# Optimization experiments

Hardware: AMD Instinct MI355X
Metric: run time of the kernel (lower is better)

Reference implementation:

```python
import jax, jax.numpy as jnp
import numpy as np

T, B, H, EMB, EVO, A = 700, 32, 800, 32, 21, 60
DIN = EMB + EVO            # 53 = embedding + evolutionary profile
RNN_OUT = 2 * H + DIN      # 1653 = bi-LSTM output + skip connection

BOND_LENGTHS = jnp.array([145.801, 152.326, 132.868], jnp.float32)
BOND_ANGLES = jnp.array([2.124, 1.941, 2.028], jnp.float32)
INIT_MAT = jnp.array([[-np.sqrt(0.5), np.sqrt(1.5), 0.0],
                      [-np.sqrt(2.0), 0.0, 0.0],
                      [0.0, 0.0, 0.0]], jnp.float32)


def setup_inputs():
    key = jax.random.key(0)
    ks = jax.random.split(key, 12)
    s = 0.03  # ~ pytorch LSTM uniform(-1/sqrt(H), 1/sqrt(H)) scale

    def lstm_params(k, d):
        k1, k2, k3 = jax.random.split(k, 3)
        return (jax.random.normal(k1, (4 * H, d)) * s,
                jax.random.normal(k2, (4 * H, H)) * s,
                jax.random.normal(k3, (4 * H,)) * s)  # b = b_ih + b_hh fused

    Wih0f, Whh0f, b0f = lstm_params(ks[0], DIN)
    Wih0b, Whh0b, b0b = lstm_params(ks[1], DIN)
    Wih1f, Whh1f, b1f = lstm_params(ks[2], 2 * H)
    Wih1b, Whh1b, b1b = lstm_params(ks[3], 2 * H)
    emb = jax.random.normal(ks[4], (21, EMB)) * s
    emb = emb.at[0].set(0.0)  # padding_idx=0
    fcW = jax.random.normal(ks[5], (A, RNN_OUT)) * s
    fcb = jax.random.normal(ks[6], (A,)) * s
    alphabet = jnp.pi * jnp.tanh(jax.random.normal(ks[7], (A, 3)))  # angularize
    primary = jax.random.randint(ks[8], (T, B), 0, 21)
    evolutionary = jax.random.normal(ks[9], (T, B, EVO))
    return {"primary": primary, "evolutionary": evolutionary, "seq_length": T,
            "emb": emb,
            "Wih0f": Wih0f, "Whh0f": Whh0f, "b0f": b0f,
            "Wih0b": Wih0b, "Whh0b": Whh0b, "b0b": b0b,
            "Wih1f": Wih1f, "Whh1f": Whh1f, "b1f": b1f,
            "Wih1b": Wih1b, "Whh1b": Whh1b, "b1b": b1b,
            "fcW": fcW, "fcb": fcb, "alphabet": alphabet}


def lstm_dir(xs, Wih, Whh, b, reverse):
    """One direction of an LSTM over xs [T, B, D] -> [T, B, H] (PyTorch gate order i,f,g,o)."""
    if reverse:
        xs = xs[::-1]
    xg = jnp.einsum('tbd,gd->tbg', xs, Wih) + b  # precompute input projection

    def step(carry, g_t):
        h, c = carry
        g = g_t + h @ Whh.T
        i, f, gg, o = jnp.split(g, 4, axis=-1)
        c = jax.nn.sigmoid(f) * c + jax.nn.sigmoid(i) * jnp.tanh(gg)
        h = jax.nn.sigmoid(o) * jnp.tanh(c)
        return (h, c), h

    z = jnp.zeros((xs.shape[1], Whh.shape[1]), xs.dtype)
    _, hs = jax.lax.scan(step, (z, z), xg)
    return hs[::-1] if reverse else hs


def dihedral_to_point(dih):
    """dih [T, B, 3] -> backbone points in local frames [3T, B, 3]."""
    rct = BOND_LENGTHS * jnp.cos(jnp.pi - BOND_ANGLES)
    rst = BOND_LENGTHS * jnp.sin(jnp.pi - BOND_ANGLES)
    px = jnp.broadcast_to(rct, dih.shape)
    pts = jnp.stack([px, jnp.cos(dih) * rst, jnp.sin(dih) * rst], axis=-1)  # [T,B,3,3]
    t, b = dih.shape[0], dih.shape[1]
    return pts.transpose(0, 2, 1, 3).reshape(3 * t, b, 3)


def point_to_coordinate(pts):
    """Sequential NeRF extension: pts [3T, B, 3] -> coords [3T, B, 3]."""
    b_sz = pts.shape[1]
    a = jnp.broadcast_to(INIT_MAT[0], (b_sz, 3))
    b = jnp.broadcast_to(INIT_MAT[1], (b_sz, 3))
    c = jnp.broadcast_to(INIT_MAT[2], (b_sz, 3))

    def norm(v):
        return v / jnp.sqrt(jnp.sum(v * v, axis=-1, keepdims=True) + 1e-12)

    def step(carry, p):
        a, b, c = carry
        bc = norm(c - b)
        n = norm(jnp.cross(b - a, bc))
        coord = c + p[:, 0:1] * bc + p[:, 1:2] * jnp.cross(n, bc) + p[:, 2:3] * n
        return (b, c, coord), coord

    _, coords = jax.lax.scan(step, (a, b, c), pts)
    return coords


def reference(primary, evolutionary, seq_length, emb,
              Wih0f, Whh0f, b0f, Wih0b, Whh0b, b0b,
              Wih1f, Whh1f, b1f, Wih1b, Whh1b, b1b,
              fcW, fcb, alphabet):
    # seq_length == T for all sequences, so packing is identity.
    x = jnp.concatenate([emb[primary], evolutionary], axis=-1)  # [T,B,53]
    h0 = jnp.concatenate([lstm_dir(x, Wih0f, Whh0f, b0f, False),
                          lstm_dir(x, Wih0b, Whh0b, b0b, True)], axis=-1)   # [T,B,1600]
    h1 = jnp.concatenate([lstm_dir(h0, Wih1f, Whh1f, b1f, False),
                          lstm_dir(h0, Wih1b, Whh1b, b1b, True)], axis=-1)  # [T,B,1600]
    out = jnp.concatenate([h1, x], axis=-1)  # skip connection -> [T,B,1653]
    logits = jnp.einsum('tbd,ad->tba', out, fcW) + fcb  # [T,B,60]
    probs = jax.nn.softmax(logits, axis=-1)  # alphabet_temperature = 1.0
    dih = jnp.arctan2(probs @ jnp.sin(alphabet), probs @ jnp.cos(alphabet))  # [T,B,3]
    return point_to_coordinate(dihedral_to_point(dih))  # [3T, B, 3]
```

## Files before the change

kernel.cpp:

```cpp
#include <hip/hip_runtime.h>
#include <hip/hip_bf16.h>
#include <math.h>


typedef unsigned int u32;
typedef unsigned long long u64;
typedef __bf16 bf16x8 __attribute__((ext_vector_type(8)));
typedef float  f32x4  __attribute__((ext_vector_type(4)));

#define TT 700
#define BT 32
#define HROW 1664
#define CH 50
#define NCH (TT / CH)
#define SLOT ((size_t)2 * CH * 3200 * 32)
#define LDS_FU (108 * 512 + 102400)

__device__ __forceinline__ f32x4 mfma16(bf16x8 a, bf16x8 b, f32x4 c) {
  return __builtin_amdgcn_mfma_f32_16x16x32_bf16(a, b, c, 0, 0, 0);
}
__device__ __forceinline__ float sigf(float x) { return 1.f / (1.f + __expf(-x)); }

#define ALOAD(p)    __hip_atomic_load((p), __ATOMIC_RELAXED, __HIP_MEMORY_SCOPE_AGENT)
#define ASTORE(p,v) __hip_atomic_store((p), (v), __ATOMIC_RELAXED, __HIP_MEMORY_SCOPE_AGENT)

__device__ __forceinline__ void lds_barrier() {
  asm volatile("s_waitcnt lgkmcnt(0)" ::: "memory");
  __builtin_amdgcn_s_barrier();
}

__device__ __forceinline__ bf16x8 cvt8(f32x4 a, f32x4 b) {
  bf16x8 r;
  r[0] = (__bf16)a[0]; r[1] = (__bf16)a[1]; r[2] = (__bf16)a[2]; r[3] = (__bf16)a[3];
  r[4] = (__bf16)b[0]; r[5] = (__bf16)b[1]; r[6] = (__bf16)b[2]; r[7] = (__bf16)b[3];
  return r;
}

#define QUAD_TRANSPOSE(l_, a0, a1, a2, a3, o0, o1, o2, o3)                   \
  {                                                                          \
    float s0 = __shfl_xor(a0, 1), s1 = __shfl_xor(a1, 1);                    \
    float s2 = __shfl_xor(a2, 1), s3 = __shfl_xor(a3, 1);                    \
    const bool e1 = ((l_) & 1) == 0;                                         \
    float n0 = e1 ? a0 : s1, n1 = e1 ? s0 : a1;                              \
    float n2 = e1 ? a2 : s3, n3 = e1 ? s2 : a3;                              \
    float t0 = __shfl_xor(n0, 2), t1 = __shfl_xor(n1, 2);                    \
    float t2 = __shfl_xor(n2, 2), t3 = __shfl_xor(n3, 2);                    \
    const bool e2 = ((l_) & 2) == 0;                                         \
    o0 = e2 ? n0 : t2; o1 = e2 ? n1 : t3;                                    \
    o2 = e2 ? t0 : n2; o3 = e2 ? t1 : n3;                                    \
  }

__global__ void pack_wx0_kernel(const float* Wih0f, const float* Wih0b, __bf16* wx0) {
  int idx = blockIdx.x * 256 + threadIdx.x;
  if (idx >= 2 * 3200 * 64) return;
  int d = idx / (3200 * 64);
  int r = (idx / 64) % 3200;
  int k = idx % 64;
  const float* W = d ? Wih0b : Wih0f;
  wx0[idx] = (k < 53) ? (__bf16)W[(size_t)r * 53 + k] : (__bf16)0.f;
}

__global__ void pack_fc_kernel(const float* fcW, __bf16* wfc) {
  int idx = blockIdx.x * 256 + threadIdx.x;
  if (idx >= 64 * 1664) return;
  int a = idx / 1664, k = idx % 1664;
  __bf16 v = (__bf16)0.f;
  if (a < 60 && k < 1653) v = (__bf16)fcW[(size_t)a * 1653 + k];
  wfc[idx] = v;
}

__global__ void xpad_kernel(const int* primary, const float* evo,
                            const float* emb, __bf16* xpad) {
  int idx = blockIdx.x * 256 + threadIdx.x;
  int t = idx >> 11;
  int b = (idx >> 6) & 31;
  int k = idx & 63;
  __bf16 v = (__bf16)0.f;
  if (k < 32)      v = (__bf16)emb[primary[t * 32 + b] * 32 + k];
  else if (k < 53) v = (__bf16)evo[((size_t)t * 32 + b) * 21 + (k - 32)];
  xpad[idx] = v;
}

__global__ void small_init_kernel(__bf16* zerobuf, u32* flags,
                                  float* sinA, float* cosA, const float* alpha) {
  int idx = blockIdx.x * 256 + threadIdx.x;
  if (idx < 32 * HROW) zerobuf[idx] = (__bf16)0.f;
  if (idx < 11392) flags[idx] = 0u;
  int j = idx - 32 * HROW;
  if (j >= 0 && j < 192) {
    if (j < 180) {
      float v = alpha[j];
      sinA[j] = sinf(v);
      cosA[j] = cosf(v);
    } else { sinA[j] = 0.f; cosA[j] = 0.f; }
  }
}

__device__ __forceinline__ void wait_lines(u32* flags, int base, int count,
                                           unsigned gen) {
  const int tid = threadIdx.x;
  if (tid < 64) {
    int spin = 0;
    for (;;) {
      bool ok = true;
      for (int j = tid; j < count; j += 64)
        ok = ok && (ALOAD(flags + (size_t)(base + j) * 32) >= gen);
      if (__popcll(__ballot(ok)) == 64) break;
      if (++spin > 24) __builtin_amdgcn_s_sleep(1);
    }
  }
  __syncthreads();
}

__device__ __forceinline__ void rec_barrier(u32* flags, unsigned gen,
                                            int base, int count) {
  asm volatile("s_waitcnt vmcnt(0)" ::: "memory");
  __syncthreads();
  if (threadIdx.x == 0) ASTORE(flags + (size_t)blockIdx.x * 32, gen);
  wait_lines(flags, base, count, gen);
}

struct FusedArgs {
  const __bf16 *xpad, *wx0, *zero;
  const float *Whh0f, *Whh0b, *b0f, *b0b;
  const float *Whh1f, *Whh1b, *Wih1f, *Wih1b, *b1f, *b1b;
  __bf16 *h0, *h1, *xg;
  u32 *f0, *f1;
  int mode;
};

__global__ __launch_bounds__(256, 1) void lstm_fused(FusedArgs A) {
  extern __shared__ __bf16 u2[];
  const int tid = threadIdx.x, w = tid >> 6, l = tid & 63;
  const int nidx = l & 15, q = l >> 4, bL = l & 31, gl = l >> 5;
  __bf16* wlds = u2 + 108 * 256;

  if (blockIdx.x < 100) {
    const int wg = blockIdx.x, d = wg / 50, u0 = (wg % 50) * 16;
    const int dcol = d * 832;
    const int row = (nidx & 3) * 800 + u0 + 4 * w + (nidx >> 2);

    {
      const float bias_n = (d ? A.b0b : A.b0f)[row];
      const float* wrf = (d ? A.Whh0b : A.Whh0f) + (size_t)row * 800 + q * 8;
#pragma unroll
      for (int sl = 0; sl < 25; ++sl) {
        f32x4 wa = *(const f32x4*)(wrf + sl * 32);
        f32x4 wb = *(const f32x4*)(wrf + sl * 32 + 4);
        *(bf16x8*)(wlds + ((size_t)(w * 25 + sl) * 64 + l) * 8) = cvt8(wa, wb);
      }
      const __bf16* wx_row = A.wx0 + (size_t)d * 3200 * 64 + (size_t)row * 64 + q * 8;
      bf16x8 wx_r0 = *(const bf16x8*)wx_row;
      bf16x8 wx_r1 = *(const bf16x8*)(wx_row + 32);
      __syncthreads();

      float cA = 0.f, cB = 0.f;
#pragma unroll 1
      for (int s = 0; s < TT; ++s) {
        const int tt = d ? (TT - 1 - s) : s;
        const __bf16* hprev =
            (s == 0) ? A.zero : (A.h0 + (size_t)(d ? tt + 1 : tt - 1) * (BT * HROW));

        bf16x8 hreg[13];
        const __bf16* hsrc = hprev + (size_t)bL * HROW + dcol;
#pragma unroll
        for (int i = 0; i < 12; ++i)
          hreg[i] = *(const bf16x8*)(hsrc + (i * 8 + w * 2 + gl) * 8);
        if (w < 2) hreg[12] = *(const bf16x8*)(hsrc + (96 + w * 2 + gl) * 8);
        bf16x8 xv = *(const bf16x8*)(A.xpad + ((size_t)tt * BT + bL) * 64 + (tid >> 5) * 8);

#pragma unroll
        for (int i = 0; i < 12; ++i)
          *(bf16x8*)(u2 + (size_t)(i * 8 + w * 2 + gl) * 256 + bL * 8) = hreg[i];
        if (w < 2)
          *(bf16x8*)(u2 + (size_t)(96 + w * 2 + gl) * 256 + bL * 8) = hreg[12];
        *(bf16x8*)(u2 + (size_t)(100 + (tid >> 5)) * 256 + bL * 8) = xv;
        __syncthreads();

        f32x4 acc0 = {0.f, 0.f, 0.f, 0.f}, acc1 = {0.f, 0.f, 0.f, 0.f};
#pragma unroll
        for (int sl = 0; sl < 27; ++sl) {
          bf16x8 bfr;
          if (sl < 25)
            bfr = *(const bf16x8*)(wlds + ((size_t)(w * 25 + sl) * 64 + l) * 8);
          else
            bfr = (sl == 25) ? wx_r0 : wx_r1;
          const __bf16* ab = u2 + (size_t)(sl * 4 + q) * 256 + nidx * 8;
          bf16x8 a0 = *(const bf16x8*)ab;
          bf16x8 a1 = *(const bf16x8*)(ab + 128);
          acc0 = mfma16(a0, bfr, acc0);
          acc1 = mfma16(a1, bfr, acc1);
        }

        {
          float a0 = acc0[0] + bias_n, a1 = acc0[1] + bias_n,
                a2 = acc0[2] + bias_n, a3 = acc0[3] + bias_n;
          float e0 = acc1[0] + bias_n, e1v = acc1[1] + bias_n,
                e2v = acc1[2] + bias_n, e3 = acc1[3] + bias_n;
          float iA, fA, gA, oA, iB, fB, gB, oB;
          QUAD_TRANSPOSE(l, a0, a1, a2, a3, iA, fA, gA, oA);
          QUAD_TRANSPOSE(l, e0, e1v, e2v, e3, iB, fB, gB, oB);
          cA = sigf(fA) * cA + sigf(iA) * tanhf(gA);
          float hA = sigf(oA) * tanhf(cA);
          cB = sigf(fB) * cB + sigf(iB) * tanhf(gB);
          float hB = sigf(oB) * tanhf(cB);
          float hA2 = __shfl_xor(hA, 4);
          float hB2 = __shfl_xor(hB, 4);
          if ((l & 4) == 0) {
            const int bA = q * 4 + (nidx & 3);
            const int colp = dcol + u0 + 4 * w + (nidx >> 2);
            union { u32 u; __bf16 h2[2]; } pk;
            pk.h2[0] = (__bf16)hA; pk.h2[1] = (__bf16)hA2;
            ASTORE((u32*)(A.h0 + ((size_t)tt * BT + bA) * HROW + colp), pk.u);
            pk.h2[0] = (__bf16)hB; pk.h2[1] = (__bf16)hB2;
            ASTORE((u32*)(A.h0 + ((size_t)tt * BT + bA + 16) * HROW + colp), pk.u);
          }
        }

        if (s < TT - 1) rec_barrier(A.f0, (unsigned)(s + 1), d * 50, 50);
      }

      asm volatile("s_waitcnt vmcnt(0)" ::: "memory");
      __syncthreads();
      if (tid == 0) ASTORE(A.f0 + (size_t)wg * 32, (unsigned)TT);
    }

    {
      const int POS1[14]  = {2, 3, 4, 5, 6, 7, 0, 1, 8, 9, 10, 11, 12, 13};
      const int SLOT1[14] = {2, 3, 2, 3, 2, 3, 0, 1, 2, 3, 0, 1, 2, 3};
      const float* wrf = (d ? A.Whh1b : A.Whh1f) + (size_t)row * 800 + q * 8;
      __syncthreads();
#pragma unroll
      for (int sl = 0; sl < 25; ++sl) {
        f32x4 wa = *(const f32x4*)(wrf + sl * 32);
        f32x4 wb = *(const f32x4*)(wrf + sl * 32 + 4);
        *(bf16x8*)(wlds + ((size_t)(w * 25 + sl) * 64 + l) * 8) = cvt8(wa, wb);
      }
      __syncthreads();
      float cA = 0.f, cB = 0.f;

      for (int k = 0; k < NCH; ++k) {
        const int pos = A.mode ? POS1[k] : k;
        wait_lines(A.f1, 100, 156, (unsigned)(pos + 1));
        const int slot = A.mode ? SLOT1[k] : (k & 1);
        const __bf16* buf = A.xg + (size_t)slot * SLOT;
        const u64* xga0 = (const u64*)(buf + ((size_t)(d * CH) * 3200 + row) * 32 + q * 4);
        u64 x0 = ALOAD(xga0);
        u64 x1 = ALOAD(xga0 + 4);
#pragma unroll 1
        for (int si = 0; si < CH; ++si) {
          const int s = k * CH + si;
          const int tt = d ? (TT - 1 - s) : s;
          const __bf16* hprev =
              (s == 0) ? A.zero
                       : (A.h1 + (size_t)(d ? tt + 1 : tt - 1) * (BT * HROW));

          u64 cx0 = x0, cx1 = x1;
          if (si + 1 < CH) {
            const u64* xgn = (const u64*)(buf +
                ((size_t)(d * CH + si + 1) * 3200 + row) * 32 + q * 4);
            x0 = ALOAD(xgn);
            x1 = ALOAD(xgn + 4);
          }

          bf16x8 hreg[13];
          const __bf16* hsrc = hprev + (size_t)bL * HROW + dcol;
#pragma unroll
          for (int i = 0; i < 12; ++i)
            hreg[i] = *(const bf16x8*)(hsrc + (i * 8 + w * 2 + gl) * 8);
          if (w < 2) hreg[12] = *(const bf16x8*)(hsrc + (96 + w * 2 + gl) * 8);

          union { u64 u; __bf16 h[4]; } ux0, ux1;
          ux0.u = cx0; ux1.u = cx1;
          f32x4 acc0 = {(float)ux0.h[0], (float)ux0.h[1],
                        (float)ux0.h[2], (float)ux0.h[3]};
          f32x4 acc1 = {(float)ux1.h[0], (float)ux1.h[1],
                        (float)ux1.h[2], (float)ux1.h[3]};

#pragma unroll
          for (int i = 0; i < 12; ++i)
            *(bf16x8*)(u2 + (size_t)(i * 8 + w * 2 + gl) * 256 + bL * 8) = hreg[i];
          if (w < 2)
            *(bf16x8*)(u2 + (size_t)(96 + w * 2 + gl) * 256 + bL * 8) = hreg[12];
          lds_barrier();

#pragma unroll
          for (int sl = 0; sl < 25; ++sl) {
            bf16x8 bfr = *(const bf16x8*)(wlds + ((size_t)(w * 25 + sl) * 64 + l) * 8);
            const __bf16* ab = u2 + (size_t)(sl * 4 + q) * 256 + nidx * 8;
            bf16x8 a0 = *(const bf16x8*)ab;
            bf16x8 a1 = *(const bf16x8*)(ab + 128);
            acc0 = mfma16(a0, bfr, acc0);
            acc1 = mfma16(a1, bfr, acc1);
          }

          {
            float a0 = acc0[0], a1 = acc0[1], a2 = acc0[2], a3 = acc0[3];
            float e0 = acc1[0], e1v = acc1[1], e2v = acc1[2], e3 = acc1[3];
            float iA, fA, gA, oA, iB, fB, gB, oB;
            QUAD_TRANSPOSE(l, a0, a1, a2, a3, iA, fA, gA, oA);
            QUAD_TRANSPOSE(l, e0, e1v, e2v, e3, iB, fB, gB, oB);
            cA = sigf(fA) * cA + sigf(iA) * tanhf(gA);
            float hA = sigf(oA) * tanhf(cA);
            cB = sigf(fB) * cB + sigf(iB) * tanhf(gB);
            float hB = sigf(oB) * tanhf(cB);
            float hA2 = __shfl_xor(hA, 4);
            float hB2 = __shfl_xor(hB, 4);
            if ((l & 4) == 0) {
              const int bA = q * 4 + (nidx & 3);
              const int colp = dcol + u0 + 4 * w + (nidx >> 2);
              union { u32 u; __bf16 h2[2]; } pk;
              pk.h2[0] = (__bf16)hA; pk.h2[1] = (__bf16)hA2;
              ASTORE((u32*)(A.h1 + ((size_t)tt * BT + bA) * HROW + colp), pk.u);
              pk.h2[0] = (__bf16)hB; pk.h2[1] = (__bf16)hB2;
              ASTORE((u32*)(A.h1 + ((size_t)tt * BT + bA + 16) * HROW + colp), pk.u);
            }
          }

          if (s < TT - 1) rec_barrier(A.f1, (unsigned)(s + 1), 0 + d * 50, 50);
        }
      }
    }
  } else {
    const int P1[14]    = {6, 7, 0, 1, 2, 3, 4, 5, 8, 9, 10, 11, 12, 13};
    const int WAIT1[14] = {-1,-1,-1,-1, 0, 1, 2, 3, 4, 5, 6, 7, 8, 9};
    const int SLOT1[14] = {2, 3, 2, 3, 2, 3, 0, 1, 2, 3, 0, 1, 2, 3};
    const int g = blockIdx.x - 100;
    const int u_begin = (g * 400) / 156;
    const int u_end   = ((g + 1) * 400) / 156;
    const int nslots  = (u_end - u_begin) * 50;
    const int rh = w >> 1, bh = w & 1;

    bf16x8 pre[13];
    f32x4 acc = {0.f, 0.f, 0.f, 0.f};
    int cur_tl = -1;
    float bn = 0.f;
    int rr = 0;

    for (int ki = 0; ki < NCH; ++ki) {
      const int k = A.mode ? P1[ki] : ki;
      {
        const int n1 = (k + 1) * CH, n2 = TT - k * CH;
        wait_lines(A.f0, 0, 100, (unsigned)(n1 > n2 ? n1 : n2));
      }
      const int wc = A.mode ? WAIT1[ki] : (ki - 2);
      if (wc >= 0) wait_lines(A.f1, 0, 100, (unsigned)((wc + 1) * CH));
      __bf16* buf = A.xg + (size_t)(A.mode ? SLOT1[k] : (k & 1)) * SLOT;

      {
        const int th0 = u_begin & 1;
        const int dir0 = (u_begin >> 1) / 100;
        const int tloc0 = th0 * 25;
        const int t0 = dir0 ? (TT - 1 - k * CH - tloc0) : (k * CH + tloc0);
        const __bf16* hs = A.h0 + ((size_t)t0 * BT + bL) * HROW;
#pragma unroll
        for (int i = 0; i < 12; ++i)
          pre[i] = *(const bf16x8*)(hs + (i * 8 + w * 2 + gl) * 8);
        if (w < 2) pre[12] = *(const bf16x8*)(hs + (96 + w * 2 + gl) * 8);
      }

#pragma unroll 1
      for (int s = 0; s < nslots; ++s) {
        const int u = u_begin + s / 50;
        const int r = s % 50;
        const int tl = u >> 1, th = u & 1;
        const int tloc = th * 25 + (r >> 1);
        const int pass = r & 1;
        const int dir = tl / 100, rt = tl % 100;
        const int rbase = rt * 32;

        if (tl != cur_tl) {
          cur_tl = tl;
          const float* W = dir ? A.Wih1b : A.Wih1f;
          __syncthreads();
          for (int i = w * 25; i < w * 25 + 25; ++i) {
            const int rhh = i / 50, sl = i % 50;
            const int rrr = rbase + rhh * 16 + nidx;
            const float* wp = W + (size_t)rrr * 1600 + sl * 32 + q * 8;
            f32x4 wa = *(const f32x4*)wp;
            f32x4 wb = *(const f32x4*)(wp + 4);
            *(bf16x8*)(wlds + ((size_t)i * 64 + l) * 8) = cvt8(wa, wb);
          }
          __syncthreads();
          rr = rbase + rh * 16 + nidx;
          bn = (dir ? A.b1b : A.b1f)[rr];
        }

#pragma unroll
        for (int i = 0; i < 12; ++i)
          *(bf16x8*)(u2 + (size_t)(i * 8 + w * 2 + gl) * 256 + bL * 8) = pre[i];
        if (w < 2)
          *(bf16x8*)(u2 + (size_t)(96 + w * 2 + gl) * 256 + bL * 8) = pre[12];
        lds_barrier();

        if (s + 1 < nslots) {
          const int s2 = s + 1;
          const int un = u_begin + s2 / 50;
          const int r2 = s2 % 50;
          const int thn = un & 1;
          const int tlocn = thn * 25 + (r2 >> 1);
          const int passn = r2 & 1;
          const int dirn = (un >> 1) / 100;
          const int tn = dirn ? (TT - 1 - k * CH - tlocn) : (k * CH + tlocn);
          const __bf16* hs = A.h0 + ((size_t)tn * BT + bL) * HROW + passn * 832;
#pragma unroll
          for (int i = 0; i < 12; ++i)
            pre[i] = *(const bf16x8*)(hs + (i * 8 + w * 2 + gl) * 8);
          if (w < 2) pre[12] = *(const bf16x8*)(hs + (96 + w * 2 + gl) * 8);
        }
        __builtin_amdgcn_sched_barrier(0);

        if (pass == 0) acc = f32x4{0.f, 0.f, 0.f, 0.f};
#pragma unroll
        for (int sl = 0; sl < 25; ++sl) {
          bf16x8 b = *(const bf16x8*)(wlds +
              ((size_t)(rh * 50 + pass * 25 + sl) * 64 + l) * 8);
          bf16x8 a = *(const bf16x8*)(u2 +
              (size_t)(sl * 4 + q) * 256 + (bh * 16 + nidx) * 8);
          acc = mfma16(a, b, acc);
        }
        lds_barrier();

        if (pass == 1) {
          union { u64 u; __bf16 h[4]; } pv;
#pragma unroll
          for (int r2 = 0; r2 < 4; ++r2) pv.h[r2] = (__bf16)(acc[r2] + bn);
          ASTORE((u64*)(buf + ((size_t)(dir * CH + tloc) * 3200 + rr) * 32 +
                        bh * 16 + q * 4), pv.u);
        }
      }
      asm volatile("s_waitcnt vmcnt(0)" ::: "memory");
      __syncthreads();
      if (tid == 0) ASTORE(A.f1 + (size_t)(100 + g) * 32, (unsigned)(ki + 1));
    }
  }
}

__global__ __launch_bounds__(256) void fc_kernel(
    const __bf16* __restrict__ h1, const __bf16* __restrict__ xpad,
    const __bf16* __restrict__ wfc, const float* __restrict__ fcb,
    const float* __restrict__ sinA, const float* __restrict__ cosA,
    float* __restrict__ pts) {
  __shared__ float lg[32 * 64];
  const int t = blockIdx.x, tid = threadIdx.x;
  const int wave = tid >> 6, lane = tid & 63, nidx = lane & 15, q = lane >> 4;
  const int a_col = wave * 16 + nidx;
  const __bf16* wrow = wfc + (size_t)a_col * 1664 + q * 8;
  const __bf16* h1row = h1 + (size_t)t * BT * HROW;
  const __bf16* xrow  = xpad + (size_t)t * BT * 64;
  f32x4 acc0 = {0.f, 0.f, 0.f, 0.f}, acc1 = {0.f, 0.f, 0.f, 0.f};
#pragma unroll
  for (int sl = 0; sl < 52; ++sl) {
    const int k = sl * 32 + q * 8;
    bf16x8 a0, a1;
    if (sl < 50) {
      const int kp = (sl < 25) ? k : (k + 32);
      a0 = *(const bf16x8*)(h1row + (size_t)nidx * HROW + kp);
      a1 = *(const bf16x8*)(h1row + (size_t)(16 + nidx) * HROW + kp);
    } else {
      a0 = *(const bf16x8*)(xrow + nidx * 64 + (k - 1600));
      a1 = *(const bf16x8*)(xrow + (16 + nidx) * 64 + (k - 1600));
    }
    bf16x8 bfr = *(const bf16x8*)(wrow + sl * 32);
    acc0 = mfma16(a0, bfr, acc0);
    acc1 = mfma16(a1, bfr, acc1);
  }
  const float bn = (a_col < 60) ? fcb[a_col] : -1e30f;
#pragma unroll
  for (int r = 0; r < 4; ++r) {
    lg[(q * 4 + r) * 64 + a_col]      = acc0[r] + bn;
    lg[(16 + q * 4 + r) * 64 + a_col] = acc1[r] + bn;
  }
  __syncthreads();

  const int b = tid >> 3, j = tid & 7;
  float v[8];
  float m = -1e30f;
#pragma unroll
  for (int k2 = 0; k2 < 8; ++k2) {
    v[k2] = lg[b * 64 + j + 8 * k2];
    m = fmaxf(m, v[k2]);
  }
  m = fmaxf(m, __shfl_xor(m, 1, 8));
  m = fmaxf(m, __shfl_xor(m, 2, 8));
  m = fmaxf(m, __shfl_xor(m, 4, 8));
  float s = 0.f;
#pragma unroll
  for (int k2 = 0; k2 < 8; ++k2) { v[k2] = __expf(v[k2] - m); s += v[k2]; }
  s += __shfl_xor(s, 1, 8);
  s += __shfl_xor(s, 2, 8);
  s += __shfl_xor(s, 4, 8);
  const float inv = 1.f / s;
  float ps[3] = {0.f, 0.f, 0.f}, pc[3] = {0.f, 0.f, 0.f};
#pragma unroll
  for (int k2 = 0; k2 < 8; ++k2) {
    const int a = j + 8 * k2;
    const float p = v[k2] * inv;
#pragma unroll
    for (int c = 0; c < 3; ++c) {
      ps[c] += p * sinA[a * 3 + c];
      pc[c] += p * cosA[a * 3 + c];
    }
  }
#pragma unroll
  for (int c = 0; c < 3; ++c) {
    ps[c] += __shfl_xor(ps[c], 1, 8);
    ps[c] += __shfl_xor(ps[c], 2, 8);
    ps[c] += __shfl_xor(ps[c], 4, 8);
    pc[c] += __shfl_xor(pc[c], 1, 8);
    pc[c] += __shfl_xor(pc[c], 2, 8);
    pc[c] += __shfl_xor(pc[c], 4, 8);
  }
  if (j == 0) {
    const float BL[3] = {145.801f, 152.326f, 132.868f};
    const float BA[3] = {2.124f, 1.941f, 2.028f};
#pragma unroll
    for (int c = 0; c < 3; ++c) {
      const float ang = 3.14159265358979323846f - BA[c];
      const float rct = BL[c] * cosf(ang), rst = BL[c] * sinf(ang);
      const float dih = atan2f(ps[c], pc[c]);
      float* o = pts + ((size_t)(3 * t + c) * BT + b) * 3;
      o[0] = rct;
      o[1] = cosf(dih) * rst;
      o[2] = sinf(dih) * rst;
    }
  }
}

__global__ void nerf_kernel(const float* __restrict__ pts, float* __restrict__ out) {
  const int b = threadIdx.x;
  if (b >= 32) return;
  float ax = -0.70710678f, ay = 1.22474487f, az = 0.f;
  float bx = -1.41421356f, by = 0.f, bz = 0.f;
  float cx = 0.f, cy = 0.f, cz = 0.f;
#pragma unroll 4
  for (int i = 0; i < 3 * TT; ++i) {
    const float* p = pts + ((size_t)i * BT + b) * 3;
    const float p0 = p[0], p1 = p[1], p2 = p[2];
    float ux = cx - bx, uy = cy - by, uz = cz - bz;
    const float ri = rsqrtf(ux * ux + uy * uy + uz * uz + 1e-12f);
    ux *= ri; uy *= ri; uz *= ri;
    const float wx = bx - ax, wy = by - ay, wz = bz - az;
    float nx = wy * uz - wz * uy, ny = wz * ux - wx * uz, nz = wx * uy - wy * ux;
    const float rn = rsqrtf(nx * nx + ny * ny + nz * nz + 1e-12f);
    nx *= rn; ny *= rn; nz *= rn;
    const float mx = ny * uz - nz * uy, my = nz * ux - nx * uz, mz = nx * uy - ny * ux;
    const float ox = cx + p0 * ux + p1 * mx + p2 * nx;
    const float oy = cy + p0 * uy + p1 * my + p2 * ny;
    const float oz = cz + p0 * uz + p1 * mz + p2 * nz;
    out[((size_t)i * BT + b) * 3 + 0] = ox;
    out[((size_t)i * BT + b) * 3 + 1] = oy;
    out[((size_t)i * BT + b) * 3 + 2] = oz;
    ax = bx; ay = by; az = bz;
    bx = cx; by = cy; bz = cz;
    cx = ox; cy = oy; cz = oz;
  }
}

extern "C" void kernel_launch(void* const* d_in, const int* in_sizes, int n_in,
                              void* d_out, int out_size, void* d_ws, size_t ws_size,
                              hipStream_t stream) {
  (void)in_sizes; (void)n_in; (void)out_size;
  const int*   primary = (const int*)d_in[0];
  const float* evo     = (const float*)d_in[1];
  const float* emb     = (const float*)d_in[3];
  const float* Wih0f   = (const float*)d_in[4];
  const float* Whh0f   = (const float*)d_in[5];
  const float* b0f     = (const float*)d_in[6];
  const float* Wih0b   = (const float*)d_in[7];
  const float* Whh0b   = (const float*)d_in[8];
  const float* b0b     = (const float*)d_in[9];
  const float* Wih1f   = (const float*)d_in[10];
  const float* Whh1f   = (const float*)d_in[11];
  const float* b1f     = (const float*)d_in[12];
  const float* Wih1b   = (const float*)d_in[13];
  const float* Whh1b   = (const float*)d_in[14];
  const float* b1b     = (const float*)d_in[15];
  const float* fcW     = (const float*)d_in[16];
  const float* fcb     = (const float*)d_in[17];
  const float* alpha   = (const float*)d_in[18];

  auto al = [](size_t n) { return (n + 511) & ~(size_t)511; };
  const size_t slotB = SLOT * 2;
  const size_t fixedB =
      al((size_t)TT * BT * 64 * 2) + al((size_t)BT * HROW * 2) +
      al((size_t)2 * 3200 * 64 * 2) + al((size_t)64 * 1664 * 2) +
      al(192 * 4) + al(192 * 4) + al((size_t)3 * TT * BT * 3 * 4) +
      al(11392 * 4) + 2 * al((size_t)TT * BT * HROW * 2);
  int slots = 4, mode = 1;
  if (fixedB + al((size_t)4 * slotB) > ws_size) { slots = 2; mode = 0; }

  char* ws = (char*)d_ws;
  size_t off = 0;
  auto take = [&](size_t n) -> void* {
    void* p = ws + off;
    off += (n + 511) & ~(size_t)511;
    return p;
  };
  __bf16* xpad = (__bf16*)take((size_t)TT * BT * 64 * 2);
  __bf16* zb   = (__bf16*)take((size_t)BT * HROW * 2);
  __bf16* wx0  = (__bf16*)take((size_t)2 * 3200 * 64 * 2);
  __bf16* wfc  = (__bf16*)take((size_t)64 * 1664 * 2);
  float*  sinA = (float*)take(192 * 4);
  float*  cosA = (float*)take(192 * 4);
  float*  pts  = (float*)take((size_t)3 * TT * BT * 3 * 4);
  u32*    flags0 = (u32*)take(11392 * 4);
  u32*    flags1 = flags0 + 3200;
  __bf16* xg   = (__bf16*)take((size_t)slots * slotB);
  __bf16* h0   = (__bf16*)take((size_t)TT * BT * HROW * 2);
  __bf16* h1   = (__bf16*)take((size_t)TT * BT * HROW * 2);
  if (off > ws_size) return;

  static int lds_cfg = 0;
  if (!lds_cfg) {
    hipFuncSetAttribute((const void*)lstm_fused,
                        hipFuncAttributeMaxDynamicSharedMemorySize, LDS_FU);
    lds_cfg = 1;
  }

  pack_wx0_kernel<<<1600, 256, 0, stream>>>(Wih0f, Wih0b, wx0);
  pack_fc_kernel<<<(64 * 1664 + 255) / 256, 256, 0, stream>>>(fcW, wfc);
  xpad_kernel<<<(TT * BT * 64) / 256, 256, 0, stream>>>(primary, evo, emb, xpad);
  small_init_kernel<<<209, 256, 0, stream>>>(zb, flags0, sinA, cosA, alpha);

  FusedArgs fa;
  fa.xpad = xpad; fa.wx0 = wx0; fa.zero = zb;
  fa.Whh0f = Whh0f; fa.Whh0b = Whh0b; fa.b0f = b0f; fa.b0b = b0b;
  fa.Whh1f = Whh1f; fa.Whh1b = Whh1b;
  fa.Wih1f = Wih1f; fa.Wih1b = Wih1b;
  fa.b1f = b1f; fa.b1b = b1b;
  fa.h0 = h0; fa.h1 = h1; fa.xg = xg;
  fa.f0 = flags0; fa.f1 = flags1;
  fa.mode = mode;
  lstm_fused<<<256, 256, LDS_FU, stream>>>(fa);

  fc_kernel<<<TT, 256, 0, stream>>>(h1, xpad, wfc, fcb, sinA, cosA, pts);
  nerf_kernel<<<1, 64, 0, stream>>>(pts, (float*)d_out);
}
```

Before: 8.477 ms.

## Add five-slot xg buffering schedule and rotate projection work assignment per chunk

When the workspace allows, a 5-slot staging buffer is used for the layer-1 input projections. The producer and consumer chunk order and wait schedule are rewritten so more chunks can be precomputed while layer 0 is still running. The projection workgroups also rotate their unit assignment per chunk, (g + ki*67) % 156, to spread load imbalance. The cost is more workspace and a more intricate dependency schedule, where a slot-reuse error would give wrong results.

After: 8.696 ms. +2.6%, slower.

```diff
diff --git a/kernel.cpp b/kernel.cpp
--- a/kernel.cpp
+++ b/kernel.cpp
@@ -226,8 +226,10 @@
     }
 
     {
-      const int POS1[14]  = {2, 3, 4, 5, 6, 7, 0, 1, 8, 9, 10, 11, 12, 13};
-      const int SLOT1[14] = {2, 3, 2, 3, 2, 3, 0, 1, 2, 3, 0, 1, 2, 3};
+      const int POS5[14]  = {3, 4, 5, 6, 7, 2, 0, 1, 8, 9, 10, 11, 12, 13};
+      const int SLOT5[14] = {3, 4, 3, 4, 3, 2, 0, 1, 4, 3, 4, 3, 4, 3};
+      const int POS4[14]  = {2, 3, 4, 5, 6, 7, 0, 1, 8, 9, 10, 11, 12, 13};
+      const int SLOT4[14] = {2, 3, 2, 3, 2, 3, 0, 1, 2, 3, 0, 1, 2, 3};
       const float* wrf = (d ? A.Whh1b : A.Whh1f) + (size_t)row * 800 + q * 8;
       __syncthreads();
 #pragma unroll
@@ -240,9 +242,11 @@
       float cA = 0.f, cB = 0.f;
 
       for (int k = 0; k < NCH; ++k) {
-        const int pos = A.mode ? POS1[k] : k;
+        int pos, slot;
+        if (A.mode == 5)      { pos = POS5[k]; slot = SLOT5[k]; }
+        else if (A.mode == 4) { pos = POS4[k]; slot = SLOT4[k]; }
+        else                  { pos = k;       slot = k & 1;    }
         wait_lines(A.f1, 100, 156, (unsigned)(pos + 1));
-        const int slot = A.mode ? SLOT1[k] : (k & 1);
         const __bf16* buf = A.xg + (size_t)slot * SLOT;
         const u64* xga0 = (const u64*)(buf + ((size_t)(d * CH) * 3200 + row) * 32 + q * 4);
         u64 x0 = ALOAD(xga0);
@@ -322,13 +326,13 @@
       }
     }
   } else {
-    const int P1[14]    = {6, 7, 0, 1, 2, 3, 4, 5, 8, 9, 10, 11, 12, 13};
-    const int WAIT1[14] = {-1,-1,-1,-1, 0, 1, 2, 3, 4, 5, 6, 7, 8, 9};
-    const int SLOT1[14] = {2, 3, 2, 3, 2, 3, 0, 1, 2, 3, 0, 1, 2, 3};
+    const int P5[14]    = {6, 7, 5, 0, 1, 2, 3, 4, 8, 9, 10, 11, 12, 13};
+    const int WAIT5[14] = {-1,-1,-1,-1,-1, 0, 1, 2, 3, 4, 8, 9, 10, 11};
+    const int SLOT5c[14]= {3, 4, 3, 4, 3, 2, 0, 1, 4, 3, 4, 3, 4, 3};
+    const int P4[14]    = {6, 7, 0, 1, 2, 3, 4, 5, 8, 9, 10, 11, 12, 13};
+    const int WAIT4[14] = {-1,-1,-1,-1, 0, 1, 2, 3, 4, 5, 6, 7, 8, 9};
+    const int SLOT4c[14]= {2, 3, 2, 3, 2, 3, 0, 1, 2, 3, 0, 1, 2, 3};
     const int g = blockIdx.x - 100;
-    const int u_begin = (g * 400) / 156;
-    const int u_end   = ((g + 1) * 400) / 156;
-    const int nslots  = (u_end - u_begin) * 50;
     const int rh = w >> 1, bh = w & 1;
 
     bf16x8 pre[13];
@@ -338,14 +342,21 @@
     int rr = 0;
 
     for (int ki = 0; ki < NCH; ++ki) {
-      const int k = A.mode ? P1[ki] : ki;
+      int k, wc, slot;
+      if (A.mode == 5)      { k = P5[ki]; wc = WAIT5[ki]; slot = SLOT5c[k]; }
+      else if (A.mode == 4) { k = P4[ki]; wc = WAIT4[ki]; slot = SLOT4c[k]; }
+      else                  { k = ki;     wc = ki - 2;    slot = ki & 1;    }
+      const int gg = (g + ki * 67) % 156;
+      const int u_begin = (gg * 400) / 156;
+      const int u_end   = ((gg + 1) * 400) / 156;
+      const int nslots  = (u_end - u_begin) * 50;
+
       {
         const int n1 = (k + 1) * CH, n2 = TT - k * CH;
         wait_lines(A.f0, 0, 100, (unsigned)(n1 > n2 ? n1 : n2));
       }
-      const int wc = A.mode ? WAIT1[ki] : (ki - 2);
       if (wc >= 0) wait_lines(A.f1, 0, 100, (unsigned)((wc + 1) * CH));
-      __bf16* buf = A.xg + (size_t)(A.mode ? SLOT1[k] : (k & 1)) * SLOT;
+      __bf16* buf = A.xg + (size_t)slot * SLOT;
 
       {
         const int th0 = u_begin & 1;
@@ -587,8 +598,10 @@
       al((size_t)2 * 3200 * 64 * 2) + al((size_t)64 * 1664 * 2) +
       al(192 * 4) + al(192 * 4) + al((size_t)3 * TT * BT * 3 * 4) +
       al(11392 * 4) + 2 * al((size_t)TT * BT * HROW * 2);
-  int slots = 4, mode = 1;
-  if (fixedB + al((size_t)4 * slotB) > ws_size) { slots = 2; mode = 0; }
+  int slots, mode;
+  if (fixedB + al((size_t)5 * slotB) <= ws_size)      { slots = 5; mode = 5; }
+  else if (fixedB + al((size_t)4 * slotB) <= ws_size) { slots = 4; mode = 4; }
+  else                                                { slots = 2; mode = 2; }
 
   char* ws = (char*)d_ws;
   size_t off = 0;
```
